# Optimization experiments

Measured on AMD Instinct MI355X. Metric: run time of the kernel, lower is better.

The kernel has to match this reference:

```python
import jax, jax.numpy as jnp
import numpy as np

V, E_DIM, H_DIR, D_A, C = 50000, 300, 512, 512, 8921  # vocab, embed dim, LSTM hidden per dir, attn dim, classes
B, S = 8, 2048
RNN = 2 * H_DIR  # bidirectional output dim = rnn_dim = 1024


def setup_inputs() -> dict:
    key = jax.random.key(0)
    ks = jax.random.split(key, 13)
    sc = lambda k, shape, s=0.05: (jax.random.normal(k, shape, jnp.float32) * s)
    return {
        "text": jax.random.randint(ks[0], (B, S), 0, V),
        "length": jnp.full((B,), S, dtype=jnp.int32),  # full-length seqs: packing is identity
        "embed": sc(ks[1], (V, E_DIM), 0.1),
        # PyTorch LSTM params, gate order (i, f, g, o); bias folded: b = b_ih + b_hh
        "Wih_f": sc(ks[2], (4 * H_DIR, E_DIM)),
        "Whh_f": sc(ks[3], (4 * H_DIR, H_DIR)),
        "b_f": sc(ks[4], (4 * H_DIR,)),
        "Wih_b": sc(ks[5], (4 * H_DIR, E_DIM)),
        "Whh_b": sc(ks[6], (4 * H_DIR, H_DIR)),
        "b_b": sc(ks[7], (4 * H_DIR,)),
        "Ww": sc(ks[8], (D_A, RNN)),   # self.W: Linear(rnn_dim, d_a, bias=False)
        "Qw": sc(ks[9], (C, D_A)),     # self.Q: Linear(d_a, num_classes, bias=False)
        "Ow": sc(ks[10], (C, RNN)),    # self.output.weight
        "Ob": sc(ks[11], (C,)),        # self.output.bias
    }


def _lstm(x_sbe, Wih, Whh, b, reverse):
    # x_sbe: [S, B, E]; returns hidden states [S, B, H]
    xw = jnp.einsum('sbe,ge->sbg', x_sbe, Wih) + b  # precompute input projections [S,B,4H]
    H = Whh.shape[1]
    Bsz = x_sbe.shape[1]

    def step(carry, g_in):
        h, c = carry
        g = g_in + h @ Whh.T
        i, f, gg, o = jnp.split(g, 4, axis=-1)
        c = jax.nn.sigmoid(f) * c + jax.nn.sigmoid(i) * jnp.tanh(gg)
        h = jax.nn.sigmoid(o) * jnp.tanh(c)
        return (h, c), h

    init = (jnp.zeros((Bsz, H), x_sbe.dtype), jnp.zeros((Bsz, H), x_sbe.dtype))
    _, hs = jax.lax.scan(step, init, xw, reverse=reverse)
    return hs


def reference(text, length, embed, Wih_f, Whh_f, b_f, Wih_b, Whh_b, b_b, Ww, Qw, Ow, Ob):
    # Embedding (eval mode: dropout is identity)
    x = embed[text]                                   # [B,S,E]
    xs = jnp.swapaxes(x, 0, 1)                        # [S,B,E]
    hf = _lstm(xs, Wih_f, Whh_f, b_f, reverse=False)  # [S,B,H]
    hb = _lstm(xs, Wih_b, Whh_b, b_b, reverse=True)   # [S,B,H]
    H = jnp.swapaxes(jnp.concatenate([hf, hb], axis=-1), 0, 1)  # [B,S,rnn_dim]
    # Label-wise attention
    Z = jnp.tanh(jnp.einsum('bsd,ad->bsa', H, Ww))    # [B,S,d_a]
    scores = jnp.einsum('ca,bsa->bcs', Qw, Z)         # [B,C,S]
    alpha = jax.nn.softmax(scores, axis=2)            # softmax over seq
    E = jnp.einsum('bcs,bsd->bcd', alpha, H)          # [B,C,rnn_dim]
    logits = jnp.einsum('cd,bcd->bc', Ow, E) + Ob     # [B,C]
    return logits, alpha
```

## Files before the change

### kernel.cpp

```cpp
#include <hip/hip_runtime.h>
#include <hip/hip_bf16.h>

typedef __attribute__((ext_vector_type(4))) float f32x4;
typedef __attribute__((ext_vector_type(8))) short s16x8;
typedef __attribute__((ext_vector_type(4))) short s16x4;

#define DI __device__ __forceinline__

static constexpr int B_ = 8, S_ = 2048, E_ = 300, EP_ = 320, HD_ = 512, G4_ = 2048;
static constexpr int C_ = 8921, RNN_ = 1024, NROW_ = 16384;

DI float bf2f(unsigned short u){ unsigned int x = ((unsigned int)u) << 16; return __builtin_bit_cast(float, x); }
DI unsigned short f2bf(float f){
  unsigned int x = __builtin_bit_cast(unsigned int, f);
  x += 0x7fff + ((x >> 16) & 1);
  return (unsigned short)(x >> 16);
}
DI float sigm(float x){ return 1.f / (1.f + __expf(-x)); }
DI float tanh_f(float x){
  x = fminf(fmaxf(x, -15.f), 15.f);
  float e = __expf(2.f * x);
  return (e - 1.f) / (e + 1.f);
}
DI void gload16(const void* g, void* l){
  __builtin_amdgcn_global_load_lds((const __attribute__((address_space(1))) void*)g,
                                   (__attribute__((address_space(3))) void*)l, 16, 0, 0);
}
DI unsigned has_sent(unsigned x){
  return (unsigned)(((x & 0xFFFFu) == 0xFFFFu) | ((x >> 16) == 0xFFFFu));
}

__global__ void k_cvt_pad(const float* __restrict__ src, unsigned short* __restrict__ dst,
                          int Rs, int Cs, int Cd){
  int r = blockIdx.x;
  long db = (long)r * Cd;
  for (int c = threadIdx.x; c < Cd; c += blockDim.x){
    float v = (r < Rs && c < Cs) ? src[(long)r * Cs + c] : 0.f;
    dst[db + c] = f2bf(v);
  }
}

__global__ void k_embed(const int* __restrict__ text, const float* __restrict__ emb,
                        unsigned short* __restrict__ xe){
  int m = blockIdx.x;
  int s = m >> 3, b = m & 7;
  int tok = text[b * S_ + s];
  const float* e = emb + (long)tok * E_;
  long db = (long)m * EP_;
  for (int c = threadIdx.x; c < EP_; c += blockDim.x){
    float v = (c < E_) ? e[c] : 0.f;
    xe[db + c] = f2bf(v);
  }
}

template<int EPI>
__global__ __launch_bounds__(256, 2)
void k_gemm_bt(const unsigned short* __restrict__ A, const unsigned short* __restrict__ Bt,
               void* __restrict__ Cout, int N, int K, int Mreal,
               long aBatch, long bBatch, long cBatch, const float* __restrict__ bias){
  __shared__ unsigned short As[128 * 32];
  __shared__ unsigned short Bs[128 * 32];
  const int tid = threadIdx.x, lane = tid & 63, wid = tid >> 6;
  const int wm = wid >> 1, wn = wid & 1;
  const int bm0 = blockIdx.y * 128, bn0 = blockIdx.x * 128;
  A  += (long)blockIdx.z * aBatch;
  Bt += (long)blockIdx.z * bBatch;

  f32x4 acc[4][4];
#pragma unroll
  for (int i = 0; i < 4; ++i)
#pragma unroll
    for (int jx = 0; jx < 4; ++jx) acc[i][jx] = f32x4{0.f, 0.f, 0.f, 0.f};

  for (int k0 = 0; k0 < K; k0 += 32){
    __syncthreads();
#pragma unroll
    for (int cc = 0; cc < 2; ++cc){
      int e = tid + cc * 256;
      int row = e >> 2, seg = e & 3;
      const unsigned short* ga = A + ((long)(bm0 + row)) * K + k0 + seg * 8;
      gload16(ga, (char*)As + cc * 4096 + wid * 1024);
      const unsigned short* gb = Bt + ((long)(bn0 + row)) * K + k0 + seg * 8;
      gload16(gb, (char*)Bs + cc * 4096 + wid * 1024);
    }
    __syncthreads();
    s16x8 af[4], bfr[4];
#pragma unroll
    for (int mt = 0; mt < 4; ++mt){
      int arow = wm * 64 + mt * 16 + (lane & 15);
      af[mt] = *(const s16x8*)((const char*)As + arow * 64 + (lane >> 4) * 16);
    }
#pragma unroll
    for (int nt = 0; nt < 4; ++nt){
      int brow = wn * 64 + nt * 16 + (lane & 15);
      bfr[nt] = *(const s16x8*)((const char*)Bs + brow * 64 + (lane >> 4) * 16);
    }
#pragma unroll
    for (int mt = 0; mt < 4; ++mt)
#pragma unroll
      for (int nt = 0; nt < 4; ++nt)
        acc[mt][nt] = __builtin_amdgcn_mfma_f32_16x16x32_bf16(af[mt], bfr[nt], acc[mt][nt], 0, 0, 0);
  }

  long co = (long)blockIdx.z * cBatch;
#pragma unroll
  for (int mt = 0; mt < 4; ++mt){
#pragma unroll
    for (int r = 0; r < 4; ++r){
      int row = bm0 + wm * 64 + mt * 16 + (lane >> 4) * 4 + r;
      if (row < Mreal){
#pragma unroll
        for (int nt = 0; nt < 4; ++nt){
          int col = bn0 + wn * 64 + nt * 16 + (lane & 15);
          float v = acc[mt][nt][r];
          long idx = co + (long)row * N + col;
          if constexpr (EPI == 0) ((float*)Cout)[idx] = v;
          else if constexpr (EPI == 1) ((unsigned short*)Cout)[idx] = f2bf(tanh_f(v));
          else if constexpr (EPI == 2) ((unsigned short*)Cout)[idx] = f2bf(v + bias[col]);
          else ((unsigned short*)Cout)[idx] = f2bf(v);
        }
      }
    }
  }
}

__global__ __launch_bounds__(256, 1)
void k_lstm(const unsigned short* __restrict__ xw_all,
            const float* __restrict__ Whh_f, const float* __restrict__ Whh_b,
            unsigned short* __restrict__ Hb){
  __shared__ unsigned short hA[16 * 512];
  __shared__ float gl[4 * 8 * 40];
  char* hAc = (char*)hA;
  const int tid = threadIdx.x, lane = tid & 63, wave = tid >> 6;
  const int wg = blockIdx.x;
  const int dir = wg >> 4, w16 = wg & 15;
  const int j0 = w16 * 32;
  const float* Whh = dir ? Whh_b : Whh_f;
  const unsigned short* xw = xw_all + (long)dir * NROW_ * G4_;

  const int b_own = lane >> 3, jj = lane & 7;
  const int j_own = j0 + wave * 8 + jj;

  s16x8 Bf0[16], Bf1[16];
  {
    int c = lane & 15;
    int jd = j0 + wave * 8 + (c & 7);
    int kg = (lane >> 4) * 8;
    const float* r0 = Whh + (long)(((c < 8) ? 0 : 512) + jd) * 512;
    const float* r1 = Whh + (long)(((c < 8) ? 1024 : 1536) + jd) * 512;
#pragma unroll
    for (int kt = 0; kt < 16; ++kt){
      s16x8 v0, v1;
#pragma unroll
      for (int i = 0; i < 8; ++i){
        v0[i] = (short)f2bf(r0[kt * 32 + kg + i]);
        v1[i] = (short)f2bf(r1[kt * 32 + kg + i]);
      }
      Bf0[kt] = v0; Bf1[kt] = v1;
    }
  }
  for (int i = tid; i < 16 * 512; i += 256) hA[i] = 0;

  const int s0 = dir ? (S_ - 1) : 0;

  float creg = 0.f;
  float xwi, xwf, xwg, xwo;
  {
    long base = ((long)s0 * 8 + b_own) * G4_ + j_own;
    xwi = bf2f(xw[base]); xwf = bf2f(xw[base + 512]);
    xwg = bf2f(xw[base + 1024]); xwo = bf2f(xw[base + 1536]);
  }
  const int bp0 = tid >> 6, seg0 = tid & 63;
  const int lds0 = (bp0 * 1024 + seg0 * 16) ^ ((bp0 & 7) << 4);
  const int lds1 = ((bp0 + 4) * 1024 + seg0 * 16) ^ (((bp0 + 4) & 7) << 4);

  float* glw = gl + wave * (8 * 40);
  const int c0 = lane & 15;
  const int bb = (lane >> 4) * 4;
  const int woff = (c0 >> 3) * 10 + (c0 & 7);
  __syncthreads();

  for (int t = 0; t < S_; ++t){
    int s = dir ? (S_ - 1 - t) : t;
    float gi, gf, gg, go;
    if (t == 0){
      gi = xwi; gf = xwf; gg = xwg; go = xwo;
    } else {
      int sp = dir ? (s + 1) : (s - 1);
      const uint4* gp0 = (const uint4*)(Hb + ((long)bp0 * S_ + sp) * RNN_ + dir * HD_) + seg0;
      const uint4* gp1 = (const uint4*)(Hb + ((long)(bp0 + 4) * S_ + sp) * RNN_ + dir * HD_) + seg0;
      uint4 va0, va1;
      for (;;){
        asm volatile("global_load_dwordx4 %0, %2, off sc0 sc1\n\t"
                     "global_load_dwordx4 %1, %3, off sc0 sc1\n\t"
                     "s_waitcnt vmcnt(0)"
                     : "=&v"(va0), "=&v"(va1) : "v"(gp0), "v"(gp1) : "memory");
        unsigned bad = has_sent(va0.x) | has_sent(va0.y) | has_sent(va0.z) | has_sent(va0.w)
                     | has_sent(va1.x) | has_sent(va1.y) | has_sent(va1.z) | has_sent(va1.w);
        if (!bad) break;
      }
      __builtin_amdgcn_sched_barrier(0);
      *(uint4*)(hAc + lds0) = va0;
      *(uint4*)(hAc + lds1) = va1;
      __syncthreads();

      f32x4 q0 = {0.f,0.f,0.f,0.f}, q1 = q0, q2 = q0, q3 = q0, q4 = q0, q5 = q0, q6 = q0, q7 = q0;
      {
        int arow = lane & 15;
        int sw = (arow & 7) << 4;
        int kg16 = (lane >> 4) * 16;
#pragma unroll
        for (int kt = 0; kt < 16; kt += 4){
          int ab0 = (arow * 1024 + kt * 64 + kg16) ^ sw;
          int ab1 = (arow * 1024 + (kt + 1) * 64 + kg16) ^ sw;
          int ab2 = (arow * 1024 + (kt + 2) * 64 + kg16) ^ sw;
          int ab3 = (arow * 1024 + (kt + 3) * 64 + kg16) ^ sw;
          s16x8 f0 = *(const s16x8*)(hAc + ab0);
          s16x8 f1 = *(const s16x8*)(hAc + ab1);
          s16x8 f2 = *(const s16x8*)(hAc + ab2);
          s16x8 f3 = *(const s16x8*)(hAc + ab3);
          q0 = __builtin_amdgcn_mfma_f32_16x16x32_bf16(f0, Bf0[kt], q0, 0, 0, 0);
          q1 = __builtin_amdgcn_mfma_f32_16x16x32_bf16(f0, Bf1[kt], q1, 0, 0, 0);
          q2 = __builtin_amdgcn_mfma_f32_16x16x32_bf16(f1, Bf0[kt + 1], q2, 0, 0, 0);
          q3 = __builtin_amdgcn_mfma_f32_16x16x32_bf16(f1, Bf1[kt + 1], q3, 0, 0, 0);
          q4 = __builtin_amdgcn_mfma_f32_16x16x32_bf16(f2, Bf0[kt + 2], q4, 0, 0, 0);
          q5 = __builtin_amdgcn_mfma_f32_16x16x32_bf16(f2, Bf1[kt + 2], q5, 0, 0, 0);
          q6 = __builtin_amdgcn_mfma_f32_16x16x32_bf16(f3, Bf0[kt + 3], q6, 0, 0, 0);
          q7 = __builtin_amdgcn_mfma_f32_16x16x32_bf16(f3, Bf1[kt + 3], q7, 0, 0, 0);
        }
      }
      f32x4 acc0 = (q0 + q2) + (q4 + q6), acc1 = (q1 + q3) + (q5 + q7);
      if (lane < 32){
#pragma unroll
        for (int r = 0; r < 4; ++r){
          glw[(bb + r) * 40 + woff] = acc0[r];
          glw[(bb + r) * 40 + 20 + woff] = acc1[r];
        }
      }
      gi = glw[b_own * 40 + jj]      + xwi;
      gf = glw[b_own * 40 + 10 + jj] + xwf;
      gg = glw[b_own * 40 + 20 + jj] + xwg;
      go = glw[b_own * 40 + 30 + jj] + xwo;
    }
    creg = sigm(gf) * creg + sigm(gi) * tanh_f(gg);
    float hv = sigm(go) * tanh_f(creg);
    unsigned short* hp = Hb + ((long)b_own * S_ + s) * RNN_ + dir * HD_ + j_own;
    unsigned hd = (unsigned)f2bf(hv);
    asm volatile("global_store_short %0, %1, off sc0 sc1"
                 :: "v"(hp), "v"(hd) : "memory");
    if (t + 1 < S_){
      int sn = dir ? (s - 1) : (s + 1);
      long base = ((long)sn * 8 + b_own) * G4_ + j_own;
      xwi = bf2f(xw[base]); xwf = bf2f(xw[base + 512]);
      xwg = bf2f(xw[base + 1024]); xwo = bf2f(xw[base + 1536]);
    }
  }
}

__global__ __launch_bounds__(256)
void k_softmax_logits(float* __restrict__ alpha, const unsigned short* __restrict__ HOt,
                      const float* __restrict__ Ob, float* __restrict__ logits){
  const int lane = threadIdx.x & 63, wv = threadIdx.x >> 6;
  long row = (long)blockIdx.x * 4 + wv;
  float* a = alpha + row * (long)S_;
  const unsigned short* h = HOt + row * (long)S_;
  float v[32];
  float mx = -1e30f;
#pragma unroll
  for (int jj = 0; jj < 8; ++jj){
    f32x4 t = *(const f32x4*)(a + jj * 256 + lane * 4);
#pragma unroll
    for (int r = 0; r < 4; ++r){ v[jj * 4 + r] = t[r]; mx = fmaxf(mx, t[r]); }
  }
#pragma unroll
  for (int o = 32; o > 0; o >>= 1) mx = fmaxf(mx, __shfl_xor(mx, o));
  float sum = 0.f;
#pragma unroll
  for (int i = 0; i < 32; ++i){ v[i] = __expf(v[i] - mx); sum += v[i]; }
#pragma unroll
  for (int o = 32; o > 0; o >>= 1) sum += __shfl_xor(sum, o);
  float inv = 1.f / sum;
  float dot = 0.f;
#pragma unroll
  for (int jj = 0; jj < 8; ++jj){
    s16x4 hv = *(const s16x4*)(h + jj * 256 + lane * 4);
    f32x4 av;
#pragma unroll
    for (int r = 0; r < 4; ++r){
      float al = v[jj * 4 + r] * inv;
      av[r] = al;
      dot += al * bf2f((unsigned short)hv[r]);
    }
    *(f32x4*)(a + jj * 256 + lane * 4) = av;
  }
#pragma unroll
  for (int o = 32; o > 0; o >>= 1) dot += __shfl_xor(dot, o);
  if (lane == 0){
    int c = (int)(row % C_);
    logits[row] = dot + Ob[c];
  }
}

extern "C" void kernel_launch(void* const* d_in, const int* in_sizes, int n_in,
                              void* d_out, int out_size, void* d_ws, size_t ws_size,
                              hipStream_t stream){
  const int*   text  = (const int*)d_in[0];
  const float* emb   = (const float*)d_in[2];
  const float* Wih_f = (const float*)d_in[3];
  const float* Whh_f = (const float*)d_in[4];
  const float* b_f   = (const float*)d_in[5];
  const float* Wih_b = (const float*)d_in[6];
  const float* Whh_b = (const float*)d_in[7];
  const float* b_b   = (const float*)d_in[8];
  const float* Ww    = (const float*)d_in[9];
  const float* Qw    = (const float*)d_in[10];
  const float* Ow    = (const float*)d_in[11];
  const float* Ob    = (const float*)d_in[12];

  char* ws = (char*)d_ws;
  long o = 0;
  unsigned short* wWihF = (unsigned short*)(ws + o); o += 2048L * 320 * 2;
  unsigned short* wWihB = (unsigned short*)(ws + o); o += 2048L * 320 * 2;
  unsigned short* wWw   = (unsigned short*)(ws + o); o += 512L * 1024 * 2;
  unsigned short* wQw   = (unsigned short*)(ws + o); o += 8960L * 512 * 2;
  unsigned short* wOw   = (unsigned short*)(ws + o); o += 8960L * 1024 * 2;
  unsigned short* wH    = (unsigned short*)(ws + o); o += 8L * 2048 * 1024 * 2;
  unsigned short* wZ    = (unsigned short*)(ws + o); o += 16384L * 512 * 2;
  char* regA = ws + o;
  unsigned short* wXe  = (unsigned short*)regA;
  unsigned short* wXw  = (unsigned short*)(regA + 16384L * 320 * 2);
  unsigned short* wHOt = (unsigned short*)regA;

  float* logits = (float*)d_out;
  float* alpha  = logits + 8L * C_;

  hipMemsetAsync(wH, 0xFF, 8L * 2048 * 1024 * 2, stream);
  k_cvt_pad<<<2048, 256, 0, stream>>>(Wih_f, wWihF, 2048, 300, 320);
  k_cvt_pad<<<2048, 256, 0, stream>>>(Wih_b, wWihB, 2048, 300, 320);
  k_cvt_pad<<<512,  256, 0, stream>>>(Ww, wWw, 512, 1024, 1024);
  k_cvt_pad<<<8960, 256, 0, stream>>>(Qw, wQw, 8921, 512, 512);
  k_cvt_pad<<<8960, 256, 0, stream>>>(Ow, wOw, 8921, 1024, 1024);
  k_embed<<<16384, 256, 0, stream>>>(text, emb, wXe);

  k_gemm_bt<2><<<dim3(16, 128, 1), 256, 0, stream>>>(wXe, wWihF, wXw, 2048, 320, 16384, 0, 0, 0, b_f);
  k_gemm_bt<2><<<dim3(16, 128, 1), 256, 0, stream>>>(wXe, wWihB, wXw + 16384L * 2048, 2048, 320, 16384, 0, 0, 0, b_b);

  k_lstm<<<32, 256, 0, stream>>>(wXw, Whh_f, Whh_b, wH);

  k_gemm_bt<1><<<dim3(4, 128, 1), 256, 0, stream>>>(wH, wWw, wZ, 512, 1024, 16384, 0, 0, 0, nullptr);
  k_gemm_bt<0><<<dim3(16, 70, 8), 256, 0, stream>>>(wQw, wZ, alpha, 2048, 512, C_, 0, 2048L * 512, (long)C_ * 2048, nullptr);
  k_gemm_bt<3><<<dim3(16, 70, 8), 256, 0, stream>>>(wOw, wH, wHOt, 2048, 1024, C_, 0, 2048L * 1024, (long)C_ * 2048, nullptr);

  k_softmax_logits<<<17842, 256, 0, stream>>>(alpha, wHOt, Ob, logits);
}
```

Before: 4.998 ms.

## Fuse LSTM with downstream attention GEMMs in a persistent kernel using flag polling

Adds a persistent fused kernel. 32 blocks run the bidirectional LSTM recurrence at raised priority, while 224 worker blocks poll the hidden-state buffer for sentinel clearance and compute the Z, score and output-projection GEMM tiles per 128-step sequence chunk as they become ready. A per-chunk atomic counter orders Z tiles before score tiles. The goal is to hide the attention GEMM work under the serial LSTM latency instead of running it afterwards. It risks the workers taking bandwidth and CU time from the latency-critical recurrence, and it depends on enough workspace being available, falling back to the separate kernels otherwise.

```diff
diff --git a/kernel.cpp b/kernel.cpp
--- a/kernel.cpp
+++ b/kernel.cpp
@@ -9,6 +9,8 @@
 
 static constexpr int B_ = 8, S_ = 2048, E_ = 300, EP_ = 320, HD_ = 512, G4_ = 2048;
 static constexpr int C_ = 8921, RNN_ = 1024, NROW_ = 16384;
+static constexpr int NWORK = 224;
+static constexpr int NT_Z = 512, NT_TOT = 512 + 2 * 8960;
 
 DI float bf2f(unsigned short u){ unsigned int x = ((unsigned int)u) << 16; return __builtin_bit_cast(float, x); }
 DI unsigned short f2bf(float f){
@@ -54,17 +56,13 @@
 }
 
 template<int EPI>
-__global__ __launch_bounds__(256, 2)
-void k_gemm_bt(const unsigned short* __restrict__ A, const unsigned short* __restrict__ Bt,
-               void* __restrict__ Cout, int N, int K, int Mreal,
-               long aBatch, long bBatch, long cBatch, const float* __restrict__ bias){
-  __shared__ unsigned short As[128 * 32];
-  __shared__ unsigned short Bs[128 * 32];
+DI void gemm_tile(char* smem, const unsigned short* A, const unsigned short* Bt,
+                  void* Cout, int N, int K, int Mreal, int bm0, int bn0,
+                  const float* bias){
+  unsigned short* As = (unsigned short*)smem;
+  unsigned short* Bs = (unsigned short*)(smem + 8192);
   const int tid = threadIdx.x, lane = tid & 63, wid = tid >> 6;
   const int wm = wid >> 1, wn = wid & 1;
-  const int bm0 = blockIdx.y * 128, bn0 = blockIdx.x * 128;
-  A  += (long)blockIdx.z * aBatch;
-  Bt += (long)blockIdx.z * bBatch;
 
   f32x4 acc[4][4];
 #pragma unroll
@@ -102,7 +100,6 @@
         acc[mt][nt] = __builtin_amdgcn_mfma_f32_16x16x32_bf16(af[mt], bfr[nt], acc[mt][nt], 0, 0, 0);
   }
 
-  long co = (long)blockIdx.z * cBatch;
 #pragma unroll
   for (int mt = 0; mt < 4; ++mt){
 #pragma unroll
@@ -113,30 +110,48 @@
         for (int nt = 0; nt < 4; ++nt){
           int col = bn0 + wn * 64 + nt * 16 + (lane & 15);
           float v = acc[mt][nt][r];
-          long idx = co + (long)row * N + col;
+          long idx = (long)row * N + col;
           if constexpr (EPI == 0) ((float*)Cout)[idx] = v;
           else if constexpr (EPI == 1) ((unsigned short*)Cout)[idx] = f2bf(tanh_f(v));
           else if constexpr (EPI == 2) ((unsigned short*)Cout)[idx] = f2bf(v + bias[col]);
-          else ((unsigned short*)Cout)[idx] = f2bf(v);
+          else if constexpr (EPI == 3) ((unsigned short*)Cout)[idx] = f2bf(v);
+          else {
+            unsigned short* p = (unsigned short*)Cout + idx;
+            unsigned hd = (unsigned)f2bf(tanh_f(v));
+            asm volatile("global_store_short %0, %1, off sc0 sc1"
+                         :: "v"(p), "v"(hd) : "memory");
+          }
         }
       }
     }
   }
 }
 
-__global__ __launch_bounds__(256, 1)
-void k_lstm(const unsigned short* __restrict__ xw_all,
-            const float* __restrict__ Whh_f, const float* __restrict__ Whh_b,
-            unsigned short* __restrict__ Hb){
-  __shared__ unsigned short hA[16 * 512];
-  __shared__ float gl[4 * 8 * 40];
+template<int EPI>
+__global__ __launch_bounds__(256, 2)
+void k_gemm_bt(const unsigned short* __restrict__ A, const unsigned short* __restrict__ Bt,
+               void* __restrict__ Cout, int N, int K, int Mreal,
+               long aBatch, long bBatch, long cBatch, const float* __restrict__ bias){
+  __shared__ char smem[16384];
+  void* cb;
+  if constexpr (EPI == 0) cb = (void*)((float*)Cout + (long)blockIdx.z * cBatch);
+  else cb = (void*)((unsigned short*)Cout + (long)blockIdx.z * cBatch);
+  gemm_tile<EPI>(smem, A + (long)blockIdx.z * aBatch, Bt + (long)blockIdx.z * bBatch,
+                 cb, N, K, Mreal, blockIdx.y * 128, blockIdx.x * 128, bias);
+}
+
+DI void lstm_impl(char* smem, const unsigned short* xw_all,
+                  const float* Whh_f, const float* Whh_b,
+                  unsigned short* Hb, int wg){
+  unsigned short* hA = (unsigned short*)smem;
+  float* gl = (float*)(smem + 16384);
   char* hAc = (char*)hA;
   const int tid = threadIdx.x, lane = tid & 63, wave = tid >> 6;
-  const int wg = blockIdx.x;
   const int dir = wg >> 4, w16 = wg & 15;
   const int j0 = w16 * 32;
   const float* Whh = dir ? Whh_b : Whh_f;
   const unsigned short* xw = xw_all + (long)dir * NROW_ * G4_;
+  __builtin_amdgcn_s_setprio(1);
 
   const int b_own = lane >> 3, jj = lane & 7;
   const int j_own = j0 + wave * 8 + jj;
@@ -257,6 +272,88 @@
   }
 }
 
+__global__ __launch_bounds__(256, 1)
+void k_lstm(const unsigned short* __restrict__ xw_all,
+            const float* __restrict__ Whh_f, const float* __restrict__ Whh_b,
+            unsigned short* __restrict__ Hb){
+  __shared__ char smem[21504];
+  lstm_impl(smem, xw_all, Whh_f, Whh_b, Hb, blockIdx.x);
+}
+
+DI void pollH(const unsigned short* Hb, int bz, int sx, int tid){
+  int s_lo = sx * 128, s_hi = s_lo + 127;
+  const unsigned* fp = (const unsigned*)(Hb + ((long)bz * S_ + s_hi) * RNN_) + tid;
+  const unsigned* bp = (const unsigned*)(Hb + ((long)bz * S_ + s_lo) * RNN_ + HD_) + tid;
+  for (;;){
+    unsigned a, b;
+    asm volatile("global_load_dword %0, %2, off sc0 sc1\n\t"
+                 "global_load_dword %1, %3, off sc0 sc1\n\t"
+                 "s_waitcnt vmcnt(0)"
+                 : "=&v"(a), "=&v"(b) : "v"(fp), "v"(bp) : "memory");
+    if (!(has_sent(a) | has_sent(b))) break;
+    __builtin_amdgcn_s_sleep(64);
+  }
+  __syncthreads();
+}
+
+DI void waitZ(const int* zc, int idx, int tid){
+  if (tid == 0){
+    const int* p = zc + idx;
+    for (;;){
+      int v;
+      asm volatile("global_load_dword %0, %1, off sc0 sc1\n\ts_waitcnt vmcnt(0)"
+                   : "=v"(v) : "v"(p) : "memory");
+      if (v >= 4) break;
+      __builtin_amdgcn_s_sleep(64);
+    }
+  }
+  __syncthreads();
+}
+
+__global__ __launch_bounds__(256, 2)
+void k_fused(const unsigned short* __restrict__ xw_all,
+             const float* __restrict__ Whh_f, const float* __restrict__ Whh_b,
+             unsigned short* __restrict__ Hb,
+             const unsigned short* __restrict__ wWw, const unsigned short* __restrict__ wQw,
+             const unsigned short* __restrict__ wOw,
+             unsigned short* __restrict__ wZ, float* __restrict__ alpha,
+             unsigned short* __restrict__ wHOt, int* __restrict__ zc){
+  __shared__ char smem[21504];
+  const int tid = threadIdx.x;
+  if (blockIdx.x < 32){
+    lstm_impl(smem, xw_all, Whh_f, Whh_b, Hb, blockIdx.x);
+    return;
+  }
+  const int w = blockIdx.x - 32;
+  for (int T = w; T < NT_TOT; T += NWORK){
+    if (T < NT_Z){
+      int sxo = T >> 5, rem = T & 31, bz = rem >> 2, nt = rem & 3;
+      int sx = (sxo & 1) ? 8 + (sxo >> 1) : 7 - (sxo >> 1);
+      pollH(Hb, bz, sx, tid);
+      gemm_tile<4>(smem, Hb, wWw, wZ, 512, 1024, NROW_,
+                   bz * 2048 + sx * 128, nt * 128, nullptr);
+      asm volatile("s_waitcnt vmcnt(0)" ::: "memory");
+      __syncthreads();
+      if (tid == 0) atomicAdd(&zc[bz * 16 + sx], 1);
+    } else {
+      int u = T - NT_Z, p = u >> 1, kind = u & 1;
+      int sxo = p / 560, rem = p % 560, bz = rem / 70, y = rem % 70;
+      int sx = (sxo & 1) ? 8 + (sxo >> 1) : 7 - (sxo >> 1);
+      if (kind == 0){
+        waitZ(zc, bz * 16 + sx, tid);
+        gemm_tile<0>(smem, wQw, wZ + (long)bz * 2048 * 512,
+                     (void*)(alpha + (long)bz * C_ * 2048), 2048, 512, C_,
+                     y * 128, sx * 128, nullptr);
+      } else {
+        pollH(Hb, bz, sx, tid);
+        gemm_tile<3>(smem, wOw, Hb + (long)bz * 2048 * 1024,
+                     (void*)(wHOt + (long)bz * C_ * 2048), 2048, 1024, C_,
+                     y * 128, sx * 128, nullptr);
+      }
+    }
+  }
+}
+
 __global__ __launch_bounds__(256)
 void k_softmax_logits(float* __restrict__ alpha, const unsigned short* __restrict__ HOt,
                       const float* __restrict__ Ob, float* __restrict__ logits){
@@ -319,22 +416,27 @@
 
   char* ws = (char*)d_ws;
   long o = 0;
-  unsigned short* wWihF = (unsigned short*)(ws + o); o += 2048L * 320 * 2;
-  unsigned short* wWihB = (unsigned short*)(ws + o); o += 2048L * 320 * 2;
-  unsigned short* wWw   = (unsigned short*)(ws + o); o += 512L * 1024 * 2;
-  unsigned short* wQw   = (unsigned short*)(ws + o); o += 8960L * 512 * 2;
-  unsigned short* wOw   = (unsigned short*)(ws + o); o += 8960L * 1024 * 2;
-  unsigned short* wH    = (unsigned short*)(ws + o); o += 8L * 2048 * 1024 * 2;
-  unsigned short* wZ    = (unsigned short*)(ws + o); o += 16384L * 512 * 2;
-  char* regA = ws + o;
-  unsigned short* wXe  = (unsigned short*)regA;
-  unsigned short* wXw  = (unsigned short*)(regA + 16384L * 320 * 2);
-  unsigned short* wHOt = (unsigned short*)regA;
+  auto alloc = [&](long bytes){ char* p = ws + o; o += (bytes + 255) & ~255L; return p; };
+  unsigned short* wWihF = (unsigned short*)alloc(2048L * 320 * 2);
+  unsigned short* wWihB = (unsigned short*)alloc(2048L * 320 * 2);
+  unsigned short* wWw   = (unsigned short*)alloc(512L * 1024 * 2);
+  unsigned short* wQw   = (unsigned short*)alloc(8960L * 512 * 2);
+  unsigned short* wOw   = (unsigned short*)alloc(8960L * 1024 * 2);
+  unsigned short* wH    = (unsigned short*)alloc(8L * 2048 * 1024 * 2);
+  unsigned short* wZ    = (unsigned short*)alloc(16384L * 512 * 2);
+  int* zc               = (int*)alloc(1024);
+  unsigned short* wXe   = (unsigned short*)alloc(16384L * 320 * 2);
+  unsigned short* wXw   = (unsigned short*)alloc(2L * 16384 * 2048 * 2);
+  long needMega = o + 8L * C_ * 2048 * 2;
+  bool mega = (ws_size >= (size_t)needMega);
+  unsigned short* wHOt = mega ? (unsigned short*)(ws + o)
+                              : (unsigned short*)wXe;
 
   float* logits = (float*)d_out;
   float* alpha  = logits + 8L * C_;
 
   hipMemsetAsync(wH, 0xFF, 8L * 2048 * 1024 * 2, stream);
+  hipMemsetAsync(zc, 0, 1024, stream);
   k_cvt_pad<<<2048, 256, 0, stream>>>(Wih_f, wWihF, 2048, 300, 320);
   k_cvt_pad<<<2048, 256, 0, stream>>>(Wih_b, wWihB, 2048, 300, 320);
   k_cvt_pad<<<512,  256, 0, stream>>>(Ww, wWw, 512, 1024, 1024);
@@ -345,11 +447,15 @@
   k_gemm_bt<2><<<dim3(16, 128, 1), 256, 0, stream>>>(wXe, wWihF, wXw, 2048, 320, 16384, 0, 0, 0, b_f);
   k_gemm_bt<2><<<dim3(16, 128, 1), 256, 0, stream>>>(wXe, wWihB, wXw + 16384L * 2048, 2048, 320, 16384, 0, 0, 0, b_b);
 
-  k_lstm<<<32, 256, 0, stream>>>(wXw, Whh_f, Whh_b, wH);
-
-  k_gemm_bt<1><<<dim3(4, 128, 1), 256, 0, stream>>>(wH, wWw, wZ, 512, 1024, 16384, 0, 0, 0, nullptr);
-  k_gemm_bt<0><<<dim3(16, 70, 8), 256, 0, stream>>>(wQw, wZ, alpha, 2048, 512, C_, 0, 2048L * 512, (long)C_ * 2048, nullptr);
-  k_gemm_bt<3><<<dim3(16, 70, 8), 256, 0, stream>>>(wOw, wH, wHOt, 2048, 1024, C_, 0, 2048L * 1024, (long)C_ * 2048, nullptr);
+  if (mega){
+    k_fused<<<32 + NWORK, 256, 0, stream>>>(wXw, Whh_f, Whh_b, wH,
+                                            wWw, wQw, wOw, wZ, alpha, wHOt, zc);
+  } else {
+    k_lstm<<<32, 256, 0, stream>>>(wXw, Whh_f, Whh_b, wH);
+    k_gemm_bt<1><<<dim3(4, 128, 1), 256, 0, stream>>>(wH, wWw, wZ, 512, 1024, 16384, 0, 0, 0, nullptr);
+    k_gemm_bt<0><<<dim3(16, 70, 8), 256, 0, stream>>>(wQw, wZ, alpha, 2048, 512, C_, 0, 2048L * 512, (long)C_ * 2048, nullptr);
+    k_gemm_bt<3><<<dim3(16, 70, 8), 256, 0, stream>>>(wOw, wH, wHOt, 2048, 1024, C_, 0, 2048L * 1024, (long)C_ * 2048, nullptr);
+  }
 
   k_softmax_logits<<<17842, 256, 0, stream>>>(alpha, wHOt, Ob, logits);
 }
```

Measured after the change: 5.736 ms. +14.8%, slower.
